# Optimization experiments

Measured on AMD Instinct MI355X. Metric: run time of the kernel, lower is better.

Reference implementation:

```python
import jax, jax.numpy as jnp
import numpy as np

EMBED = 768
GH = 4        # heads per group
GD = 256      # group dim = GH * head_dim
NSTEPS = 3    # n_pde_steps
DT = 0.05
HJ_H = 0.05   # Heimburg-Jackson dispersion coefficient


def _sh(u, k):
    # shift field content along sequence axis (axis=1) by k with zero boundary
    if k == 0:
        return u
    z = jnp.zeros_like(u)
    if k > 0:
        return z.at[:, k:, :].set(u[:, :-k, :])
    return z.at[:, :k, :].set(u[:, -k:, :])


def _d1(u):
    return 0.5 * (_sh(u, -1) - _sh(u, 1))


def _d2(u):
    return _sh(u, -1) - 2.0 * u + _sh(u, 1)


def _d3(u):
    return 0.5 * (_sh(u, -2) - 2.0 * _sh(u, -1) + 2.0 * _sh(u, 1) - _sh(u, 2))


def _d4(u):
    return _sh(u, -2) - 4.0 * _sh(u, -1) + 6.0 * u - 4.0 * _sh(u, 1) + _sh(u, 2)


def _attn(x, qkv_w, qkv_b, ow, ob, nh):
    # standard causal multi-head attention on one head group
    B, T, D = x.shape
    hd = D // nh
    qkv = x @ qkv_w + qkv_b                      # (B,T,3D)
    q, k, v = jnp.split(qkv, 3, axis=-1)
    heads = lambda a: a.reshape(B, T, nh, hd).transpose(0, 2, 1, 3)
    q, k, v = heads(q), heads(k), heads(v)
    s = jnp.einsum('bhqd,bhkd->bhqk', q, k) * (1.0 / np.sqrt(hd))
    causal = jnp.tril(jnp.ones((T, T), dtype=bool))
    s = jnp.where(causal, s, jnp.asarray(-1e9, s.dtype))
    p = jax.nn.softmax(s, axis=-1)
    o = jnp.einsum('bhqk,bhkd->bhqd', p, v).transpose(0, 2, 1, 3).reshape(B, T, D)
    return o @ ow + ob


def _sine_gordon(u):
    # u_tt = u_xx - sin(u), semi-implicit Euler (leapfrog-like)
    w = jnp.zeros_like(u)
    for _ in range(NSTEPS):
        w = w + DT * (_d2(u) - jnp.sin(u))
        u = u + DT * w
    return u


def _kdv(u):
    # u_t = -6 u u_x - u_xxx, explicit Euler
    for _ in range(NSTEPS):
        u = u + DT * (-6.0 * u * _d1(u) - _d3(u))
    return u


def _hj(u):
    # Heimburg-Jackson: u_tt = d_xx((c0^2 + p u + q u^2) u) - h u_xxxx
    # with c0=1, p=-1, q=1
    w = jnp.zeros_like(u)
    for _ in range(NSTEPS):
        f = u - u * u + u * u * u
        w = w + DT * (_d2(f) - HJ_H * _d4(u))
        u = u + DT * w
    return u


def setup_inputs() -> dict:
    key = jax.random.key(0)
    ks = jax.random.split(key, 16)
    s = 0.02
    d, gd = EMBED, GD
    inp = {'x': jax.random.normal(ks[0], (4, 2048, d), dtype=jnp.float32)}
    inp['in_w'] = jax.random.normal(ks[1], (d, d), jnp.float32) * s
    inp['in_b'] = jnp.zeros((d,), jnp.float32)
    for i, n in enumerate(['sg', 'kdv', 'hj']):
        inp[n + '_qkv_w'] = jax.random.normal(ks[2 + 4 * i], (gd, 3 * gd), jnp.float32) * s
        inp[n + '_qkv_b'] = jnp.zeros((3 * gd,), jnp.float32)
        inp[n + '_out_w'] = jax.random.normal(ks[3 + 4 * i], (gd, gd), jnp.float32) * s
        inp[n + '_out_b'] = jnp.zeros((gd,), jnp.float32)
    inp['out_w'] = jax.random.normal(ks[14], (d, d), jnp.float32) * s
    inp['out_b'] = jnp.zeros((d,), jnp.float32)
    return inp


def reference(x, in_w, in_b,
              sg_qkv_w, sg_qkv_b, sg_out_w, sg_out_b,
              kdv_qkv_w, kdv_qkv_b, kdv_out_w, kdv_out_b,
              hj_qkv_w, hj_qkv_b, hj_out_w, hj_out_b,
              out_w, out_b):
    h = x @ in_w + in_b
    xg = jnp.split(h, [GD, 2 * GD], axis=-1)
    sg = _sine_gordon(_attn(xg[0], sg_qkv_w, sg_qkv_b, sg_out_w, sg_out_b, GH))
    kv = _kdv(_attn(xg[1], kdv_qkv_w, kdv_qkv_b, kdv_out_w, kdv_out_b, GH))
    hj = _hj(_attn(xg[2], hj_qkv_w, hj_qkv_b, hj_out_w, hj_out_b, GH))
    out = jnp.concatenate([sg, kv, hj], axis=-1)
    return out @ out_w + out_b
```

## Files before the change

### kernel.cpp

```cpp
#include <hip/hip_runtime.h>
#include <math.h>

#define B_   4
#define T_   2048
#define D_   768
#define M_   8192
#define GD_  256
#define NH_  4
#define HD_  64

typedef short  s16x8 __attribute__((ext_vector_type(8)));
typedef __bf16 bfx8  __attribute__((ext_vector_type(8)));
typedef float  fx4   __attribute__((ext_vector_type(4)));

#define LOG2E 1.44269504088896f
#define QSCALE (0.125f * LOG2E)

__device__ __forceinline__ short f2bf(float f) {
  union { float f; unsigned u; } v; v.f = f;
  unsigned r = v.u + 0x7fffu + ((v.u >> 16) & 1u);
  return (short)(r >> 16);
}

__device__ __forceinline__ unsigned cvt_pk_bf16(float lo, float hi) {
  unsigned r;
  asm("v_cvt_pk_bf16_f32 %0, %1, %2" : "=v"(r) : "v"(lo), "v"(hi));
  return r;
}

__device__ __forceinline__ void gload16(const void* g, void* l) {
  __builtin_amdgcn_global_load_lds(
      (const __attribute__((address_space(1))) unsigned int*)g,
      (__attribute__((address_space(3))) unsigned int*)l, 16, 0, 0);
}

struct PW { const short* p0; const short* p1; const short* p2; };
struct PB { const float* p0; const float* p1; const float* p2; };
__device__ __forceinline__ const short* selw(const PW& s, int z) {
  return z == 0 ? s.p0 : (z == 1 ? s.p1 : s.p2);
}
__device__ __forceinline__ const float* selb(const PB& s, int z) {
  return z == 0 ? s.p0 : (z == 1 ? s.p1 : s.p2);
}

template<int AT, int OBF, int MODE>
__global__ __launch_bounds__(256) void gemm_mfma(
    const void* __restrict__ Avoid, long sA, int lda,
    PW Wp, PB Bp, int K,
    void* __restrict__ C, long sC, int ldc,
    void* __restrict__ xtra)
{
  __shared__ short As[2][128 * 64];
  __shared__ short Bs[2][64 * 64];

  const int z = blockIdx.z;
  const short* Ab16 = (const short*)Avoid + (long)z * sA;
  const float* Ab32 = (const float*)Avoid + (long)z * sA;
  const short* Wb = selw(Wp, z);
  const float* bb = selb(Bp, z);

  const int n0 = blockIdx.x * 64;
  const int m0 = blockIdx.y * 128;
  const int tid = threadIdx.x, lane = tid & 63, w = tid >> 6;
  const int wm = w >> 1, wn = w & 1;
  const int quad = lane >> 4, mr = lane & 15;

  fx4 acc[4][2] = {};

  auto compute = [&](const short* Ab, const short* Bb) {
#pragma unroll
    for (int ks = 0; ks < 2; ++ks) {
      const int cc = ks * 32 + quad * 8;
      const int swz = cc ^ ((mr & 7) * 8);
      bfx8 af[4], bf[2];
#pragma unroll
      for (int i = 0; i < 4; ++i)
        af[i] = *(const bfx8*)&Ab[(wm * 64 + i * 16 + mr) * 64 + swz];
#pragma unroll
      for (int j = 0; j < 2; ++j)
        bf[j] = *(const bfx8*)&Bb[(wn * 32 + j * 16 + mr) * 64 + swz];
#pragma unroll
      for (int i = 0; i < 4; ++i)
#pragma unroll
        for (int j = 0; j < 2; ++j)
          acc[i][j] = __builtin_amdgcn_mfma_f32_16x16x32_bf16(af[i], bf[j], acc[i][j], 0, 0, 0);
    }
  };

  if (AT) {
    const int r0 = tid >> 3;
    const int cs = (tid & 7) * 8;
    const int wswz = cs ^ ((r0 & 7) * 8);
    s16x8 ar[4], br[2];

    auto loadA = [&](int k0) {
#pragma unroll
      for (int gg = 0; gg < 4; ++gg) {
        const float* p = Ab32 + (long)(m0 + r0 + 32 * gg) * lda + k0 + cs;
        float4 f0 = *(const float4*)p;
        float4 f1 = *(const float4*)(p + 4);
        short o[8] = { f2bf(f0.x), f2bf(f0.y), f2bf(f0.z), f2bf(f0.w),
                       f2bf(f1.x), f2bf(f1.y), f2bf(f1.z), f2bf(f1.w) };
        ar[gg] = *(s16x8*)o;
      }
    };
    auto loadB = [&](int k0) {
#pragma unroll
      for (int hh = 0; hh < 2; ++hh)
        br[hh] = *(const s16x8*)(Wb + (long)(n0 + r0 + 32 * hh) * K + k0 + cs);
    };

    loadA(0); loadB(0);
    for (int k0 = 0; k0 < K; k0 += 64) {
#pragma unroll
      for (int gg = 0; gg < 4; ++gg)
        *(s16x8*)&As[0][(r0 + 32 * gg) * 64 + wswz] = ar[gg];
#pragma unroll
      for (int hh = 0; hh < 2; ++hh)
        *(s16x8*)&Bs[0][(r0 + 32 * hh) * 64 + wswz] = br[hh];
      __syncthreads();
      if (k0 + 64 < K) { loadA(k0 + 64); loadB(k0 + 64); }
      compute(&As[0][0], &Bs[0][0]);
      __syncthreads();
    }
  } else {
    const int lrow = lane >> 3, lcol = lane & 7;

    auto stageA = [&](short* dst, int k0) {
#pragma unroll
      for (int i = 0; i < 4; ++i) {
        const int r = i * 32 + w * 8 + lrow;
        const int swz = (lcol * 8) ^ ((r & 7) * 8);
        gload16(Ab16 + (long)(m0 + r) * lda + k0 + swz,
                dst + (i * 32 + w * 8) * 64);
      }
    };
    auto stageB = [&](short* dst, int k0) {
#pragma unroll
      for (int i = 0; i < 2; ++i) {
        const int r = i * 32 + w * 8 + lrow;
        const int swz = (lcol * 8) ^ ((r & 7) * 8);
        gload16(Wb + (long)(n0 + r) * K + k0 + swz,
                dst + (i * 32 + w * 8) * 64);
      }
    };

    stageA(&As[0][0], 0); stageB(&Bs[0][0], 0);
    const int NT = K >> 6;
    for (int t = 0; t < NT; ++t) {
      const int cur = t & 1;
      if (t + 1 < NT) {
        stageA(&As[cur ^ 1][0], (t + 1) * 64);
        stageB(&Bs[cur ^ 1][0], (t + 1) * 64);
        asm volatile("s_waitcnt vmcnt(6)" ::: "memory");
      } else {
        asm volatile("s_waitcnt vmcnt(0)" ::: "memory");
      }
      __builtin_amdgcn_s_barrier();
      compute(&As[cur][0], &Bs[cur][0]);
      __builtin_amdgcn_s_barrier();
    }
  }

  float* Cf = (float*)C + (long)z * sC;
  short* Cs = (short*)C + (long)z * sC;
#pragma unroll
  for (int j = 0; j < 2; ++j) {
    const int col = n0 + wn * 32 + j * 16 + mr;
    const float bvx = bb[col];
#pragma unroll
    for (int i = 0; i < 4; ++i) {
      const int row0 = m0 + wm * 64 + i * 16 + quad * 4;
      if (MODE == 2) {
        const int rb = row0 >> 11, t0 = row0 & 2047;
        fx4 o;
#pragma unroll
        for (int r = 0; r < 4; ++r) o[r] = acc[i][j][r] + bvx;
        *(fx4*)((float*)xtra + (((long)z * B_ + rb) * GD_ + col) * T_ + t0) = o;
      } else if (MODE == 1 && col >= 512) {
        const int h = (col - 512) >> 6, hd = (col - 512) & 63;
        const int rb = row0 >> 11, t0 = row0 & 2047;
        short o4[4];
#pragma unroll
        for (int r = 0; r < 4; ++r) o4[r] = f2bf(acc[i][j][r] + bvx);
        *(short4*)((short*)xtra + ((((long)z * B_ + rb) * NH_ + h) * HD_ + hd) * T_ + t0) =
            *(short4*)o4;
      } else {
        const float sc = (MODE == 1 && col < 256) ? QSCALE : 1.0f;
#pragma unroll
        for (int r = 0; r < 4; ++r) {
          float v = (acc[i][j][r] + bvx) * sc;
          if (OBF) Cs[(long)(row0 + r) * ldc + col] = f2bf(v);
          else     Cf[(long)(row0 + r) * ldc + col] = v;
        }
      }
    }
  }
}

__global__ __launch_bounds__(256) void flash_attn_mfma(
    short* __restrict__ qkv, const short* __restrict__ vtb)
{
  __shared__ short Ks[64][72];
  __shared__ short Vs[80][72];
  __shared__ short Ps[128 * 64];

  const int bid = blockIdx.x;
  const int Q = 15 - (bid / 48);
  const int combo = bid % 48;
  const int g = combo % 3, bh = combo / 3;
  const int b = bh >> 2, h = bh & 3;

  short* base = qkv + ((size_t)g * M_ + (size_t)b * T_) * D_;
  short*       Qp = base + h * HD_;
  const short* Kp = base + GD_ + h * HD_;
  const short* Vtp = vtb + ((((size_t)g * B_ + b) * NH_ + h) * HD_) * T_;

  const int tid = threadIdx.x, lane = tid & 63, w = tid >> 6;
  const int quad = lane >> 4, mr = lane & 15;
  const int q0 = Q * 128, wr = w * 32;
  const int qhi = q0 + wr + 31;

  const int sra = tid >> 3, sc = (tid & 7) * 8;

  if (tid < 128) {
    const short ov = 0x3F80;
    s16x8 one = { ov, ov, ov, ov, ov, ov, ov, ov };
    *(s16x8*)&Vs[64 + (tid >> 3)][(tid & 7) * 8] = one;
  }

  bfx8 aq[2][2];
#pragma unroll
  for (int f = 0; f < 2; ++f)
#pragma unroll
    for (int ks = 0; ks < 2; ++ks)
      aq[f][ks] = *(const bfx8*)(Qp + (size_t)(q0 + wr + f * 16 + mr) * D_ +
                                 ks * 32 + quad * 8);

  s16x8 kreg0 = *(const s16x8*)(Kp + (size_t)sra * D_ + sc);
  s16x8 kreg1 = *(const s16x8*)(Kp + (size_t)(sra + 32) * D_ + sc);
  s16x8 vreg0 = *(const s16x8*)(Vtp + (size_t)sra * T_ + sc);
  s16x8 vreg1 = *(const s16x8*)(Vtp + (size_t)(sra + 32) * T_ + sc);

  fx4 Oa[2][5] = {};

  char* PsB = (char*)&Ps[0];
  const int rot = (mr & 7) << 4;

  const int ktmax = 2 * Q + 1;
  for (int kt = 0; kt <= ktmax; ++kt) {
    *(s16x8*)&Ks[sra][sc]      = kreg0;
    *(s16x8*)&Ks[sra + 32][sc] = kreg1;
    *(s16x8*)&Vs[sra][sc]      = vreg0;
    *(s16x8*)&Vs[sra + 32][sc] = vreg1;
    __syncthreads();

    if (kt < ktmax) {
      const int kn = (kt + 1) * 64;
      kreg0 = *(const s16x8*)(Kp + (size_t)(kn + sra) * D_ + sc);
      kreg1 = *(const s16x8*)(Kp + (size_t)(kn + sra + 32) * D_ + sc);
      vreg0 = *(const s16x8*)(Vtp + (size_t)sra * T_ + kn + sc);
      vreg1 = *(const s16x8*)(Vtp + (size_t)(sra + 32) * T_ + kn + sc);
    }

    if (kt * 64 <= qhi) {
      fx4 st[4][2] = {};
#pragma unroll
      for (int ks = 0; ks < 2; ++ks) {
        bfx8 bk[4];
#pragma unroll
        for (int jj = 0; jj < 4; ++jj)
          bk[jj] = *(const bfx8*)&Ks[jj * 16 + mr][ks * 32 + quad * 8];
#pragma unroll
        for (int jj = 0; jj < 4; ++jj)
#pragma unroll
          for (int f = 0; f < 2; ++f)
            st[jj][f] = __builtin_amdgcn_mfma_f32_16x16x32_bf16(bk[jj], aq[f][ks], st[jj][f], 0, 0, 0);
      }

      if (kt >= 2 * Q) {
#pragma unroll
        for (int jj = 0; jj < 4; ++jj)
#pragma unroll
          for (int f = 0; f < 2; ++f) {
            const int qg = q0 + wr + f * 16 + mr;
            const int kvg0 = kt * 64 + jj * 16 + quad * 4;
#pragma unroll
            for (int r = 0; r < 4; ++r)
              if (kvg0 + r > qg) st[jj][f][r] = -1e30f;
          }
      }

#pragma unroll
      for (int f = 0; f < 2; ++f) {
        const int rowb = (wr + f * 16 + mr) << 7;
#pragma unroll
        for (int jj = 0; jj < 4; ++jj) {
          float e0 = exp2f(st[jj][f][0]);
          float e1 = exp2f(st[jj][f][1]);
          float e2 = exp2f(st[jj][f][2]);
          float e3 = exp2f(st[jj][f][3]);
          unsigned pk0 = cvt_pk_bf16(e0, e1);
          unsigned pk1 = cvt_pk_bf16(e2, e3);
          unsigned long long pv = (unsigned long long)pk0 |
                                  ((unsigned long long)pk1 << 32);
          const int kb = (jj * 32 + quad * 8) ^ rot;
          *(unsigned long long*)(PsB + rowb + kb) = pv;
        }
      }

#pragma unroll
      for (int ks = 0; ks < 2; ++ks) {
        bfx8 ap[2];
#pragma unroll
        for (int f = 0; f < 2; ++f) {
          const int rowb = (wr + f * 16 + mr) << 7;
          const int kb = (ks * 64 + quad * 16) ^ rot;
          ap[f] = *(const bfx8*)(PsB + rowb + kb);
        }
#pragma unroll
        for (int j = 0; j < 5; ++j) {
          bfx8 bv = *(const bfx8*)&Vs[j * 16 + mr][ks * 32 + quad * 8];
#pragma unroll
          for (int f = 0; f < 2; ++f)
            Oa[f][j] = __builtin_amdgcn_mfma_f32_16x16x32_bf16(ap[f], bv, Oa[f][j], 0, 0, 0);
        }
      }
    }
    __syncthreads();
  }

#pragma unroll
  for (int f = 0; f < 2; ++f)
#pragma unroll
    for (int r = 0; r < 4; ++r) {
      const float inv = 1.0f / Oa[f][4][r];
      const int row = q0 + wr + f * 16 + quad * 4 + r;
#pragma unroll
      for (int j = 0; j < 4; ++j)
        Qp[(size_t)row * D_ + j * 16 + mr] = f2bf(Oa[f][j][r] * inv);
    }
}

__device__ __forceinline__ float fhj(float x) { return x - x * x + x * x * x; }

__global__ __launch_bounds__(256) void pde_kernel(
    const float* __restrict__ ut, short* __restrict__ ubt)
{
  const int cg = blockIdx.x, b = blockIdx.y, g = blockIdx.z;
  const int tid = threadIdx.x;
  const int c = tid >> 6, lane = tid & 63;
  const int t0 = lane * 32;
  const float dt = 0.05f;

  const float* src = ut + (((size_t)g * B_ + b) * GD_ + cg * 4 + c) * T_ + t0;

  float uc[36];
#pragma unroll
  for (int q = 0; q < 8; ++q)
    *(fx4*)&uc[2 + q * 4] = *(const fx4*)(src + q * 4);

  {
    float h0 = __shfl_up(uc[32], 1);
    float h1 = __shfl_up(uc[33], 1);
    float h2 = __shfl_down(uc[2], 1);
    float h3 = __shfl_down(uc[3], 1);
    uc[0]  = (lane == 0)  ? 0.f : h0;
    uc[1]  = (lane == 0)  ? 0.f : h1;
    uc[34] = (lane == 63) ? 0.f : h2;
    uc[35] = (lane == 63) ? 0.f : h3;
  }

  float wreg[32];
#pragma unroll
  for (int i = 0; i < 32; ++i) wreg[i] = 0.f;

  for (int step = 0; step < 3; ++step) {
    float nu[32];
#pragma unroll
    for (int tt = 0; tt < 32; ++tt) {
      float um2 = uc[tt], um1 = uc[tt + 1], u = uc[tt + 2];
      float up1 = uc[tt + 3], up2 = uc[tt + 4];
      if (g == 0) {
        float d2 = up1 - 2.f * u + um1;
        wreg[tt] += dt * (d2 - __sinf(u));
        nu[tt] = u + dt * wreg[tt];
      } else if (g == 1) {
        float d1 = 0.5f * (up1 - um1);
        float d3 = 0.5f * (up2 - 2.f * up1 + 2.f * um1 - um2);
        nu[tt] = u + dt * (-6.f * u * d1 - d3);
      } else {
        float d2f = fhj(up1) - 2.f * fhj(u) + fhj(um1);
        float d4  = up2 - 4.f * up1 + 6.f * u - 4.f * um1 + um2;
        wreg[tt] += dt * (d2f - 0.05f * d4);
        nu[tt] = u + dt * wreg[tt];
      }
    }
    float h0 = __shfl_up(nu[30], 1);
    float h1 = __shfl_up(nu[31], 1);
    float h2 = __shfl_down(nu[0], 1);
    float h3 = __shfl_down(nu[1], 1);
    uc[0]  = (lane == 0)  ? 0.f : h0;
    uc[1]  = (lane == 0)  ? 0.f : h1;
    uc[34] = (lane == 63) ? 0.f : h2;
    uc[35] = (lane == 63) ? 0.f : h3;
#pragma unroll
    for (int i = 0; i < 32; ++i) uc[2 + i] = nu[i];
  }

  short o16[32];
#pragma unroll
  for (int i = 0; i < 32; ++i) o16[i] = f2bf(uc[2 + i]);
  short* dst = ubt + (((size_t)g * B_ + b) * GD_ + cg * 4 + c) * T_ + t0;
#pragma unroll
  for (int q = 0; q < 4; ++q)
    *(s16x8*)(dst + q * 8) = *(s16x8*)&o16[q * 8];
}

__global__ __launch_bounds__(256) void transp_kernel(
    const short* __restrict__ ubt, short* __restrict__ ub)
{
  __shared__ short Ls[32][264];

  const int tt = blockIdx.x;
  const int ct = blockIdx.y;
  const int z  = blockIdx.z;
  const int g = z >> 2, b = z & 3;
  const int tid = threadIdx.x;
  const int c0 = ct * 32, t0 = tt * 256;

  const short* src = ubt + (((size_t)g * B_ + b) * GD_ + c0) * T_ + t0;
#pragma unroll
  for (int it = 0; it < 4; ++it) {
    const int row = (tid >> 5) + it * 8;
    const int col = (tid & 31) * 8;
    *(s16x8*)&Ls[row][col] = *(const s16x8*)(src + (size_t)row * T_ + col);
  }
  __syncthreads();

  short* dst = ub + (size_t)b * T_ * D_ + g * GD_ + c0;
  const int cq = tid & 7, tr = tid >> 3;
#pragma unroll
  for (int p = 0; p < 8; ++p) {
    const int tl = p * 32 + tr;
    short o4[4];
#pragma unroll
    for (int i = 0; i < 4; ++i) o4[i] = Ls[cq * 4 + i][tl];
    *(short4*)(dst + (size_t)(t0 + tl) * D_ + cq * 4) = *(short4*)o4;
  }
}

struct PrepArgs {
  const float* w[8]; short* wt[8];
  int K[8], N[8];
  int tend[8];
};

__global__ __launch_bounds__(256) void prep_kernel(PrepArgs pa)
{
  const int bid = blockIdx.x, tid = threadIdx.x;
  __shared__ float Ws[32][33];
  int ti = 0;
#pragma unroll
  for (int i = 0; i < 8; ++i) if (bid >= pa.tend[i]) ti = i + 1;
  const int tloc = bid - (ti ? pa.tend[ti - 1] : 0);
  const int K = pa.K[ti], N = pa.N[ti];
  const int ntx = N >> 5;
  const int k0 = (tloc / ntx) * 32, n0 = (tloc % ntx) * 32;
  const float* W = pa.w[ti];
  short* WT = pa.wt[ti];
  const int tx = tid & 31, ty = tid >> 5;

#pragma unroll
  for (int i = 0; i < 4; ++i)
    Ws[ty + 8 * i][tx] = W[(long)(k0 + ty + 8 * i) * N + n0 + tx];
  __syncthreads();
#pragma unroll
  for (int i = 0; i < 4; ++i) {
    int r = ty + 8 * i;
    WT[(long)(n0 + r) * K + k0 + tx] = f2bf(Ws[tx][r]);
  }
}

extern "C" void kernel_launch(void* const* d_in, const int* in_sizes, int n_in,
                              void* d_out, int out_size, void* d_ws, size_t ws_size,
                              hipStream_t stream)
{
  (void)in_sizes; (void)n_in; (void)out_size; (void)ws_size;

  const float* x         = (const float*)d_in[0];
  const float* in_w      = (const float*)d_in[1];
  const float* in_b      = (const float*)d_in[2];
  const float* sg_qkv_w  = (const float*)d_in[3];
  const float* sg_qkv_b  = (const float*)d_in[4];
  const float* sg_out_w  = (const float*)d_in[5];
  const float* sg_out_b  = (const float*)d_in[6];
  const float* kdv_qkv_w = (const float*)d_in[7];
  const float* kdv_qkv_b = (const float*)d_in[8];
  const float* kdv_out_w = (const float*)d_in[9];
  const float* kdv_out_b = (const float*)d_in[10];
  const float* hj_qkv_w  = (const float*)d_in[11];
  const float* hj_qkv_b  = (const float*)d_in[12];
  const float* hj_out_w  = (const float*)d_in[13];
  const float* hj_out_b  = (const float*)d_in[14];
  const float* out_w     = (const float*)d_in[15];
  const float* out_b     = (const float*)d_in[16];
  float* out = (float*)d_out;

  const size_t MD = (size_t)M_ * D_;
  short* base = (short*)d_ws;
  short* hb   = base + MD;
  float* uf   = (float*)d_ws;
  short* qkvb = base + 2 * MD;
  short* ub16 = qkvb + 3 * MD;
  short* wts  = ub16 + MD;
  short* in_wT  = wts;
  short* qkvT0  = in_wT + 589824;
  short* qkvT1  = qkvT0 + 196608;
  short* qkvT2  = qkvT1 + 196608;
  short* outT0  = qkvT2 + 196608;
  short* outT1  = outT0 + 65536;
  short* outT2  = outT1 + 65536;
  short* out_wT = outT2 + 65536;
  short* vtb    = out_wT + 589824;
  short* ubt    = qkvb;

  dim3 blk(256);

  PrepArgs pa;
  const float* wsrc[8] = { in_w, sg_qkv_w, kdv_qkv_w, hj_qkv_w,
                           sg_out_w, kdv_out_w, hj_out_w, out_w };
  short* wdst[8] = { in_wT, qkvT0, qkvT1, qkvT2, outT0, outT1, outT2, out_wT };
  int Ksz[8] = { 768, 256, 256, 256, 256, 256, 256, 768 };
  int Nsz[8] = { 768, 768, 768, 768, 256, 256, 256, 768 };
  int cum = 0;
  for (int i = 0; i < 8; ++i) {
    pa.w[i] = wsrc[i]; pa.wt[i] = wdst[i]; pa.K[i] = Ksz[i]; pa.N[i] = Nsz[i];
    cum += (Ksz[i] >> 5) * (Nsz[i] >> 5);
    pa.tend[i] = cum;
  }
  prep_kernel<<<dim3((unsigned)cum), blk, 0, stream>>>(pa);

  gemm_mfma<1, 1, 0><<<dim3(12, 64, 1), blk, 0, stream>>>(
      x, 0, D_, PW{in_wT, in_wT, in_wT}, PB{in_b, in_b, in_b}, D_,
      hb, 0, D_, nullptr);

  gemm_mfma<0, 1, 1><<<dim3(12, 64, 3), blk, 0, stream>>>(
      hb, 256, D_,
      PW{qkvT0, qkvT1, qkvT2}, PB{sg_qkv_b, kdv_qkv_b, hj_qkv_b}, GD_,
      qkvb, (long)MD, D_, vtb);

  flash_attn_mfma<<<dim3(768), blk, 0, stream>>>(qkvb, vtb);

  gemm_mfma<0, 0, 2><<<dim3(4, 64, 3), blk, 0, stream>>>(
      qkvb, (long)MD, D_,
      PW{outT0, outT1, outT2}, PB{sg_out_b, kdv_out_b, hj_out_b}, GD_,
      uf, 0, 0, uf);

  pde_kernel<<<dim3(64, 4, 3), blk, 0, stream>>>(uf, ubt);

  transp_kernel<<<dim3(8, 8, 12), blk, 0, stream>>>(ubt, ub16);

  gemm_mfma<0, 0, 0><<<dim3(12, 64, 1), blk, 0, stream>>>(
      ub16, 0, D_, PW{out_wT, out_wT, out_wT}, PB{out_b, out_b, out_b}, D_,
      out, 0, D_, nullptr);
}
```

Measured before the change: 298.8 us.

## Double-buffer K/V tiles in LDS via direct global-to-LDS loads with XOR swizzle

Replaces the register-staged K/V prefetch, which was written into padded shared arrays, with a two-buffer LDS ring. The ring is filled by a gload16 helper that writes global data straight into LDS, and it uses an XOR-swizzled 64-wide layout in place of padding. The aim is to remove the register round-trip and the sync at the top of each iteration, letting the next tile load overlap compute. In exchange it doubles the K/V LDS footprint, which may lower occupancy. Correctness depends on the async load completing before the trailing barrier.

```diff
diff --git a/kernel.cpp b/kernel.cpp
--- a/kernel.cpp
+++ b/kernel.cpp
@@ -201,8 +201,8 @@
 __global__ __launch_bounds__(256) void flash_attn_mfma(
     short* __restrict__ qkv, const short* __restrict__ vtb)
 {
-  __shared__ short Ks[64][72];
-  __shared__ short Vs[80][72];
+  __shared__ short KsL[2][64 * 64];
+  __shared__ short VsL[2][80 * 64];
   __shared__ short Ps[128 * 64];
 
   const int bid = blockIdx.x;
@@ -221,13 +221,26 @@
   const int q0 = Q * 128, wr = w * 32;
   const int qhi = q0 + wr + 31;
 
-  const int sra = tid >> 3, sc = (tid & 7) * 8;
-
-  if (tid < 128) {
+  const int lrow = lane >> 3, lcol = lane & 7;
+  const int scsw = (lcol * 8) ^ (lrow * 8);
+
+  {
     const short ov = 0x3F80;
     s16x8 one = { ov, ov, ov, ov, ov, ov, ov, ov };
-    *(s16x8*)&Vs[64 + (tid >> 3)][(tid & 7) * 8] = one;
-  }
+    const int bufi = tid >> 7, ch = tid & 127;
+    *(s16x8*)&VsL[bufi][(64 + (ch >> 3)) * 64 + (ch & 7) * 8] = one;
+  }
+
+  auto stage = [&](int buf, int kt2) {
+    short* kd = &KsL[buf][(w * 8) * 64];
+    short* vd = &VsL[buf][(w * 8) * 64];
+    const short* kg = Kp + (size_t)(kt2 * 64 + w * 8 + lrow) * D_ + scsw;
+    const short* vg = Vtp + (size_t)(w * 8 + lrow) * T_ + kt2 * 64 + scsw;
+    gload16(kg, kd);
+    gload16(kg + (size_t)32 * D_, kd + 32 * 64);
+    gload16(vg, vd);
+    gload16(vg + (size_t)32 * T_, vd + 32 * 64);
+  };
 
   bfx8 aq[2][2];
 #pragma unroll
@@ -237,40 +250,32 @@
       aq[f][ks] = *(const bfx8*)(Qp + (size_t)(q0 + wr + f * 16 + mr) * D_ +
                                  ks * 32 + quad * 8);
 
-  s16x8 kreg0 = *(const s16x8*)(Kp + (size_t)sra * D_ + sc);
-  s16x8 kreg1 = *(const s16x8*)(Kp + (size_t)(sra + 32) * D_ + sc);
-  s16x8 vreg0 = *(const s16x8*)(Vtp + (size_t)sra * T_ + sc);
-  s16x8 vreg1 = *(const s16x8*)(Vtp + (size_t)(sra + 32) * T_ + sc);
+  stage(0, 0);
+  __syncthreads();
 
   fx4 Oa[2][5] = {};
 
   char* PsB = (char*)&Ps[0];
   const int rot = (mr & 7) << 4;
+  const int swzb = (mr & 7) * 8;
 
   const int ktmax = 2 * Q + 1;
   for (int kt = 0; kt <= ktmax; ++kt) {
-    *(s16x8*)&Ks[sra][sc]      = kreg0;
-    *(s16x8*)&Ks[sra + 32][sc] = kreg1;
-    *(s16x8*)&Vs[sra][sc]      = vreg0;
-    *(s16x8*)&Vs[sra + 32][sc] = vreg1;
-    __syncthreads();
-
-    if (kt < ktmax) {
-      const int kn = (kt + 1) * 64;
-      kreg0 = *(const s16x8*)(Kp + (size_t)(kn + sra) * D_ + sc);
-      kreg1 = *(const s16x8*)(Kp + (size_t)(kn + sra + 32) * D_ + sc);
-      vreg0 = *(const s16x8*)(Vtp + (size_t)sra * T_ + kn + sc);
-      vreg1 = *(const s16x8*)(Vtp + (size_t)(sra + 32) * T_ + kn + sc);
-    }
+    const int cur = kt & 1;
+    if (kt < ktmax) stage(cur ^ 1, kt + 1);
 
     if (kt * 64 <= qhi) {
+      const short* Kc = &KsL[cur][0];
+      const short* Vc = &VsL[cur][0];
+
       fx4 st[4][2] = {};
 #pragma unroll
       for (int ks = 0; ks < 2; ++ks) {
+        const int cc = (ks * 32 + quad * 8) ^ swzb;
         bfx8 bk[4];
 #pragma unroll
         for (int jj = 0; jj < 4; ++jj)
-          bk[jj] = *(const bfx8*)&Ks[jj * 16 + mr][ks * 32 + quad * 8];
+          bk[jj] = *(const bfx8*)&Kc[(jj * 16 + mr) * 64 + cc];
 #pragma unroll
         for (int jj = 0; jj < 4; ++jj)
 #pragma unroll
@@ -311,6 +316,7 @@
 
 #pragma unroll
       for (int ks = 0; ks < 2; ++ks) {
+        const int cc = (ks * 32 + quad * 8) ^ swzb;
         bfx8 ap[2];
 #pragma unroll
         for (int f = 0; f < 2; ++f) {
@@ -320,7 +326,7 @@
         }
 #pragma unroll
         for (int j = 0; j < 5; ++j) {
-          bfx8 bv = *(const bfx8*)&Vs[j * 16 + mr][ks * 32 + quad * 8];
+          bfx8 bv = *(const bfx8*)&Vc[(j * 16 + mr) * 64 + cc];
 #pragma unroll
           for (int f = 0; f < 2; ++f)
             Oa[f][j] = __builtin_amdgcn_mfma_f32_16x16x32_bf16(ap[f], bv, Oa[f][j], 0, 0, 0);
```

Result: no change. 300.2 us (+0.5%).
